# Kernel optimization log

Measured on AMD Instinct MI355X. Metric: run time of the kernel, lower is better.

## Reference

```python
import jax, jax.numpy as jnp
import numpy as np

N_NODES = 100000


def gcn_conv(x, W, b, src, dst, dinv):
    # PyG GCNConv with default add_self_loops=True, symmetric normalization.
    # x: [N, Fin], W: [Fin, Fout]. Self-loop contribution handled analytically
    # (norm for loop edge i->i is dinv[i]^2) instead of materializing loop edges.
    xw = x @ W                                   # [N, Fout]
    norm = dinv[src] * dinv[dst]                 # [E]
    msgs = xw[src] * norm[:, None]               # [E, Fout]
    agg = jax.ops.segment_sum(msgs, dst, num_segments=N_NODES)
    agg = agg + xw * (dinv * dinv)[:, None]      # self-loops
    return agg + b


def setup_inputs() -> dict:
    key = jax.random.key(0)
    ks = jax.random.split(key, 12)
    E = 3200000
    S = 1000000
    F_in = 512
    x = jax.random.normal(ks[0], (N_NODES, F_in), dtype=jnp.float32)
    edge_index = jax.random.randint(ks[1], (2, E), 0, N_NODES, dtype=jnp.int64)
    samples = jax.random.randint(ks[2], (S, 2), 0, N_NODES, dtype=jnp.int64)

    def glorot(k, fi, fo):
        lim = float(np.sqrt(6.0 / (fi + fo)))
        return jax.random.uniform(k, (fi, fo), jnp.float32, -lim, lim)

    W1 = glorot(ks[3], F_in, 8)
    b1 = jnp.zeros((8,), jnp.float32)
    W2 = glorot(ks[4], 8, 16)
    b2 = jnp.zeros((16,), jnp.float32)
    W3 = glorot(ks[5], 16, 32)
    b3 = jnp.zeros((32,), jnp.float32)
    Wfc = glorot(ks[6], 64, 1)
    bfc = jnp.zeros((1,), jnp.float32)
    return {"x": x, "edge_index": edge_index, "samples": samples,
            "W1": W1, "b1": b1, "W2": W2, "b2": b2, "W3": W3, "b3": b3,
            "Wfc": Wfc, "bfc": bfc}


def reference(x, edge_index, samples, W1, b1, W2, b2, W3, b3, Wfc, bfc):
    src, dst = edge_index[0], edge_index[1]
    # degree with self-loops (edge weight 1), deg >= 1 so rsqrt is safe
    deg = jax.ops.segment_sum(jnp.ones_like(src, dtype=x.dtype), dst,
                              num_segments=N_NODES) + 1.0
    dinv = jax.lax.rsqrt(deg)
    h = jax.nn.relu(gcn_conv(x, W1, b1, src, dst, dinv))
    h = jax.nn.relu(gcn_conv(h, W2, b2, src, dst, dinv))
    h = gcn_conv(h, W3, b3, src, dst, dinv)
    x_i = h[samples[:, 0]]                       # [S, 32]
    x_j = h[samples[:, 1]]                       # [S, 32]
    x_ij = jnp.concatenate([x_i, x_j], axis=1)   # [S, 64]
    return jax.nn.sigmoid(x_ij @ Wfc + bfc).squeeze(-1)
```

## Files before the change

kernel.cpp:

```cpp
#include <hip/hip_runtime.h>
#include <cstdint>

#define N_NODES 100000
#define NBKT 2048
#define KNODE 49
#define NBLK 256
#define TPB_P 512


__global__ void k_hist(const int* __restrict__ dst, int* __restrict__ hist, int E) {
    __shared__ int h[NBKT];
    for (int i = threadIdx.x; i < NBKT; i += blockDim.x) h[i] = 0;
    __syncthreads();
    int chunk = (E + NBLK - 1) / NBLK;
    int lo = blockIdx.x * chunk, hi = min(lo + chunk, E);
    for (int i = lo + threadIdx.x; i < hi; i += blockDim.x)
        atomicAdd(&h[dst[i] / KNODE], 1);
    __syncthreads();
    int* hr = hist + (size_t)blockIdx.x * NBKT;
    for (int i = threadIdx.x; i < NBKT; i += blockDim.x) hr[i] = h[i];
}


__global__ void k_offs(const int* __restrict__ hist, int* __restrict__ offs,
                       int* __restrict__ btot) {
    int bkt = blockIdx.x * blockDim.x + threadIdx.x;
    if (bkt >= NBKT) return;
    int run = 0;
    for (int rr = 0; rr < NBLK; ++rr) {
        int r = ((rr & 31) << 3) | (rr >> 5);
        int v = hist[(size_t)r * NBKT + bkt];
        offs[(size_t)r * NBKT + bkt] = run;
        run += v;
    }
    btot[bkt] = run;
}


__global__ void k_bktscan(const int* __restrict__ btot, int* __restrict__ bbase) {
    __shared__ int s[256];
    int t = threadIdx.x;
    int loc[8];
    int sum = 0;
#pragma unroll
    for (int j = 0; j < 8; ++j) { loc[j] = btot[t * 8 + j]; sum += loc[j]; }
    s[t] = sum;
    __syncthreads();
    for (int off = 1; off < 256; off <<= 1) {
        int v = (t >= off) ? s[t - off] : 0;
        __syncthreads();
        s[t] += v;
        __syncthreads();
    }
    int base = s[t] - sum;
#pragma unroll
    for (int j = 0; j < 8; ++j) { bbase[t * 8 + j] = base; base += loc[j]; }
    if (t == 255) bbase[NBKT] = base;
}


__global__ void k_place(const int* __restrict__ src, const int* __restrict__ dst,
                        const int* __restrict__ offs, const int* __restrict__ bbase,
                        int* __restrict__ tmp, int E) {
    __shared__ int cur[NBKT];
    const int* orow = offs + (size_t)blockIdx.x * NBKT;
    for (int i = threadIdx.x; i < NBKT; i += blockDim.x) cur[i] = bbase[i] + orow[i];
    __syncthreads();
    int chunk = (E + NBLK - 1) / NBLK;
    int lo = blockIdx.x * chunk, hi = min(lo + chunk, E);
    for (int i = lo + threadIdx.x; i < hi; i += blockDim.x) {
        int d = dst[i], s = src[i];
        int b = d / KNODE;
        int p = atomicAdd(&cur[b], 1);
        tmp[p] = (s << 6) | (d - b * KNODE);
    }
}


__global__ void k_countscan(const int* __restrict__ tmp, const int* __restrict__ bbase,
                            int* __restrict__ row_start, float* __restrict__ dinv, int n) {
    __shared__ int c[KNODE];
    __shared__ int p[KNODE];
    int b = blockIdx.x;
    int t = threadIdx.x;
    for (int i = t; i < KNODE; i += blockDim.x) c[i] = 0;
    __syncthreads();
    int n0 = bbase[b], n1 = bbase[b + 1];
    for (int i = n0 + t; i < n1; i += blockDim.x)
        atomicAdd(&c[tmp[i] & 63], 1);
    __syncthreads();
    if (t == 0) {
        int run = 0;
        for (int j = 0; j < KNODE; ++j) { p[j] = run; run += c[j]; }
    }
    __syncthreads();
    if (t < KNODE) {
        int node = b * KNODE + t;
        if (node < n) {
            row_start[node] = n0 + p[t];
            dinv[node] = rsqrtf((float)c[t] + 1.0f);
        }
    }
    if (b == 0 && t == 0) row_start[n] = bbase[NBKT];
}


__global__ void k_bin2(const int* __restrict__ tmp, const int* __restrict__ bbase,
                       const int* __restrict__ row_start, const float* __restrict__ dinv,
                       int2* __restrict__ csr, int n) {
    __shared__ int cur[KNODE];
    __shared__ float dd[KNODE];
    int b = blockIdx.x;
    int t = threadIdx.x;
    if (t < KNODE) {
        int node = b * KNODE + t;
        cur[t] = (node < n) ? row_start[node] : 0;
        dd[t] = (node < n) ? dinv[node] : 0.f;
    }
    __syncthreads();
    int n0 = bbase[b], n1 = bbase[b + 1];
    for (int i = n0 + t; i < n1; i += blockDim.x) {
        int e = tmp[i];
        int li = e & 63;
        int s = e >> 6;
        int pos = atomicAdd(&cur[li], 1);
        csr[pos] = make_int2(s, __float_as_int(dinv[s] * dd[li]));
    }
}


__global__ void k_gemm1(const float* __restrict__ x, const float* __restrict__ W,
                        float* __restrict__ xw, int n) {
    __shared__ float sWT[8 * 512];
    for (int i = threadIdx.x; i < 4096; i += blockDim.x) {
        int k = i >> 3, c = i & 7;
        sWT[c * 512 + k] = W[i];
    }
    __syncthreads();
    int wid = (blockIdx.x * blockDim.x + threadIdx.x) >> 6;
    int lane = threadIdx.x & 63;
    int r_sub = lane >> 3, j = lane & 7;
    int row = wid * 8 + r_sub;
    if (row >= n) return;
    const float* xr = x + (size_t)row * 512;
    float acc[8];
#pragma unroll
    for (int c = 0; c < 8; ++c) acc[c] = 0.f;
#pragma unroll 4
    for (int it = 0; it < 16; ++it) {
        int kb = it * 32 + j * 4;
        float4 v = *(const float4*)(xr + kb);
#pragma unroll
        for (int c = 0; c < 8; ++c) {
            const float* wt = &sWT[c * 512 + kb];
            acc[c] += v.x * wt[0] + v.y * wt[1] + v.z * wt[2] + v.w * wt[3];
        }
    }
#pragma unroll
    for (int off = 1; off < 8; off <<= 1)
#pragma unroll
        for (int c = 0; c < 8; ++c)
            acc[c] += __shfl_xor(acc[c], off);
    float outv = acc[0];
#pragma unroll
    for (int c = 1; c < 8; ++c) if (j == c) outv = acc[c];
    xw[(size_t)row * 8 + j] = outv;
}


__global__ void k_gather1(const float* __restrict__ xw, const int2* __restrict__ csr,
                          const int* __restrict__ row_start, const float* __restrict__ dinv,
                          const float* __restrict__ b, float* __restrict__ out, int n) {
    int wid = (blockIdx.x * blockDim.x + threadIdx.x) >> 6;
    int lane = threadIdx.x & 63;
    if (wid >= n) return;
    int e = lane >> 3, c = lane & 7;
    int k0 = row_start[wid], k1 = row_start[wid + 1];
    float acc = 0.f;
    for (int k = k0 + e; k < k1; k += 8) {
        int2 p = csr[k];
        acc += xw[(size_t)p.x * 8 + c] * __int_as_float(p.y);
    }
    if (e == 0) { float di = dinv[wid]; acc += xw[(size_t)wid * 8 + c] * di * di; }
#pragma unroll
    for (int off = 8; off < 64; off <<= 1) acc += __shfl_xor(acc, off);
    if (lane < 8) out[(size_t)wid * 8 + c] = fmaxf(acc + b[c], 0.f);
}


__global__ void k_gather2(const float* __restrict__ h1, const int2* __restrict__ csr,
                          const int* __restrict__ row_start, const float* __restrict__ dinv,
                          const float* __restrict__ W2, const float* __restrict__ b2,
                          float* __restrict__ h2, int n) {
    __shared__ float sW[8 * 16];
    __shared__ float sB[16];
    if (threadIdx.x < 128) sW[threadIdx.x] = W2[threadIdx.x];
    if (threadIdx.x < 16) sB[threadIdx.x] = b2[threadIdx.x];
    __syncthreads();
    int wid = (blockIdx.x * blockDim.x + threadIdx.x) >> 6;
    int lane = threadIdx.x & 63;
    if (wid >= n) return;
    int e = lane >> 3, c = lane & 7;
    int k0 = row_start[wid], k1 = row_start[wid + 1];
    float acc = 0.f;
    for (int k = k0 + e; k < k1; k += 8) {
        int2 p = csr[k];
        acc += h1[(size_t)p.x * 8 + c] * __int_as_float(p.y);
    }
    if (e == 0) { float di = dinv[wid]; acc += h1[(size_t)wid * 8 + c] * di * di; }
#pragma unroll
    for (int off = 8; off < 64; off <<= 1) acc += __shfl_xor(acc, off);
    float s2[8];
#pragma unroll
    for (int k = 0; k < 8; ++k) s2[k] = __shfl(acc, k);
    if (lane < 16) {
        float a = sB[lane];
#pragma unroll
        for (int k = 0; k < 8; ++k) a += s2[k] * sW[k * 16 + lane];
        h2[(size_t)wid * 16 + lane] = fmaxf(a, 0.f);
    }
}


__global__ void k_gather3(const float* __restrict__ h2, const int2* __restrict__ csr,
                          const int* __restrict__ row_start, const float* __restrict__ dinv,
                          const float* __restrict__ v, const float* __restrict__ ch,
                          float* __restrict__ pi, float* __restrict__ pj, int n) {
    int wid = (blockIdx.x * blockDim.x + threadIdx.x) >> 6;
    int lane = threadIdx.x & 63;
    if (wid >= n) return;
    int e = lane >> 4, c = lane & 15;
    int k0 = row_start[wid], k1 = row_start[wid + 1];
    float acc = 0.f;
    for (int k = k0 + e; k < k1; k += 4) {
        int2 p = csr[k];
        acc += h2[(size_t)p.x * 16 + c] * __int_as_float(p.y);
    }
    if (e == 0) { float di = dinv[wid]; acc += h2[(size_t)wid * 16 + c] * di * di; }
#pragma unroll
    for (int off = 16; off < 64; off <<= 1) acc += __shfl_xor(acc, off);
    float t = acc * v[c];
    float u = acc * v[16 + c];
#pragma unroll
    for (int off = 1; off < 16; off <<= 1) {
        t += __shfl_xor(t, off);
        u += __shfl_xor(u, off);
    }
    if (lane == 0) { pi[wid] = t + ch[0]; pj[wid] = u + ch[1]; }
}


__global__ void k_prep_head(const float* __restrict__ W3, const float* __restrict__ b3,
                            const float* __restrict__ Wfc, float* __restrict__ v,
                            float* __restrict__ c) {
    int t = threadIdx.x;
    if (t < 32) {
        int j = t & 15;
        const float* wf = Wfc + (t < 16 ? 0 : 32);
        float a = 0.f;
        for (int k = 0; k < 32; ++k) a += W3[j * 32 + k] * wf[k];
        v[t] = a;
    } else if (t < 34) {
        const float* wf = Wfc + (t == 32 ? 0 : 32);
        float a = 0.f;
        for (int k = 0; k < 32; ++k) a += b3[k] * wf[k];
        c[t - 32] = a;
    }
}


__global__ void k_samples_fast(const int2* __restrict__ samples, const float* __restrict__ pi,
                               const float* __restrict__ pj, const float* __restrict__ bfc,
                               float* __restrict__ out, int S) {
    int i = blockIdx.x * blockDim.x + threadIdx.x;
    if (i >= S) return;
    int2 s = samples[i];
    float z = pi[s.x] + pj[s.y] + bfc[0];
    out[i] = 1.0f / (1.0f + __expf(-z));
}


extern "C" void kernel_launch(void* const* d_in, const int* in_sizes, int n_in,
                              void* d_out, int out_size, void* d_ws, size_t ws_size,
                              hipStream_t stream) {
    const float* x   = (const float*)d_in[0];
    const int*   ei  = (const int*)d_in[1];
    const int*   smp = (const int*)d_in[2];
    const float* W1  = (const float*)d_in[3];
    const float* b1  = (const float*)d_in[4];
    const float* W2  = (const float*)d_in[5];
    const float* b2  = (const float*)d_in[6];
    const float* W3  = (const float*)d_in[7];
    const float* b3  = (const float*)d_in[8];
    const float* Wfc = (const float*)d_in[9];
    const float* bfc = (const float*)d_in[10];
    float* out = (float*)d_out;

    const int E = in_sizes[1] / 2;
    const int S = in_sizes[2] / 2;
    const int N = N_NODES;
    const int* src = ei;
    const int* dst = ei + E;

    char* w = (char*)d_ws;
    size_t off = 0;
    auto alloc = [&](size_t bytes) {
        char* p = w + off;
        off += (bytes + 255) & ~(size_t)255;
        return p;
    };
    int*   row_start = (int*)alloc((N + 1) * 4);
    float* dinv      = (float*)alloc(N * 4);
    int2*  csr       = (int2*)alloc((size_t)E * 8);
    int*   btot      = (int*)alloc(NBKT * 4);
    int*   bbase     = (int*)alloc((NBKT + 1) * 4);

    size_t off_layers = off;
    float* xw1       = (float*)alloc((size_t)N * 8 * 4);
    float* h1        = (float*)alloc((size_t)N * 8 * 4);
    float* h2        = (float*)alloc((size_t)N * 16 * 4);
    float* vhead     = (float*)alloc(32 * 4);
    float* chead     = (float*)alloc(2 * 4);
    float* pi        = (float*)alloc(N * 4);
    float* pj        = (float*)alloc(N * 4);

    size_t tmp_off  = off_layers;
    size_t hist_off = tmp_off + (((size_t)E * 4 + 255) & ~(size_t)255);
    size_t offs_off = hist_off + (((size_t)NBLK * NBKT * 4 + 255) & ~(size_t)255);
    int* tmp  = (int*)(w + tmp_off);
    int* hist = (int*)(w + hist_off);
    int* offs = (int*)(w + offs_off);
    size_t scratch_end = offs_off + (size_t)NBLK * NBKT * 4;
    if (scratch_end > off) off = (scratch_end + 255) & ~(size_t)255;

    dim3 B(256);
    const int GN = (N * 64 + 255) / 256;

    k_hist<<<dim3(NBLK), dim3(TPB_P), 0, stream>>>(dst, hist, E);
    k_offs<<<dim3((NBKT + 255) / 256), B, 0, stream>>>(hist, offs, btot);
    k_bktscan<<<dim3(1), B, 0, stream>>>(btot, bbase);
    k_place<<<dim3(NBLK), dim3(TPB_P), 0, stream>>>(src, dst, offs, bbase, tmp, E);
    k_countscan<<<dim3(NBKT), B, 0, stream>>>(tmp, bbase, row_start, dinv, N);
    k_bin2<<<dim3(NBKT), B, 0, stream>>>(tmp, bbase, row_start, dinv, csr, N);

    k_gemm1<<<dim3(((N + 7) / 8 * 64 + 255) / 256), B, 0, stream>>>(x, W1, xw1, N);
    k_gather1<<<dim3(GN), B, 0, stream>>>(xw1, csr, row_start, dinv, b1, h1, N);

    k_gather2<<<dim3(GN), B, 0, stream>>>(h1, csr, row_start, dinv, W2, b2, h2, N);

    k_prep_head<<<dim3(1), dim3(64), 0, stream>>>(W3, b3, Wfc, vhead, chead);
    k_gather3<<<dim3(GN), B, 0, stream>>>(h2, csr, row_start, dinv, vhead, chead, pi, pj, N);

    k_samples_fast<<<dim3((S + 255) / 256), B, 0, stream>>>((const int2*)smp, pi, pj, bfc, out, S);
}
```

Baseline: 638.4 us.

## Fold symmetric normalization into node features and drop per-edge weights from CSR

The per-edge norm dinv[s]*dinv[d] is factored: source features are pre-scaled by dinv when produced (in the GEMM and at each layer output), and the aggregate is scaled by dinv of the destination. This lets the CSR hold only 4-byte source indices instead of int2 (index, weight), halving edge-list traffic in all three gather passes and removing the dinv[s] random read at build time. The count and bin kernels are merged into one finalize kernel that caches bucket entries in shared memory, and the per-bucket offset scan is parallelised across a wavefront with shuffles. The cost is an extra multiply per node and reliance on the bucket size fitting the shared cache, with a fallback to global reads when it does not.

```diff
diff --git a/kernel.cpp b/kernel.cpp
--- a/kernel.cpp
+++ b/kernel.cpp
@@ -6,6 +6,7 @@
 #define KNODE 49
 #define NBLK 256
 #define TPB_P 512
+#define CAP  2048
 
 
 __global__ void k_hist(const int* __restrict__ dst, int* __restrict__ hist, int E) {
@@ -24,16 +25,33 @@
 
 __global__ void k_offs(const int* __restrict__ hist, int* __restrict__ offs,
                        int* __restrict__ btot) {
-    int bkt = blockIdx.x * blockDim.x + threadIdx.x;
+    int bkt = (blockIdx.x * blockDim.x + threadIdx.x) >> 6;
     if (bkt >= NBKT) return;
-    int run = 0;
-    for (int rr = 0; rr < NBLK; ++rr) {
+    int lane = threadIdx.x & 63;
+    int vals[4], loc[4];
+    int s = 0;
+#pragma unroll
+    for (int j = 0; j < 4; ++j) {
+        int rr = lane * 4 + j;
         int r = ((rr & 31) << 3) | (rr >> 5);
-        int v = hist[(size_t)r * NBKT + bkt];
-        offs[(size_t)r * NBKT + bkt] = run;
-        run += v;
-    }
-    btot[bkt] = run;
+        vals[j] = hist[(size_t)r * NBKT + bkt];
+        loc[j] = s;
+        s += vals[j];
+    }
+    int inc = s;
+#pragma unroll
+    for (int off = 1; off < 64; off <<= 1) {
+        int u = __shfl_up(inc, off);
+        if (lane >= off) inc += u;
+    }
+    int excl = inc - s;
+#pragma unroll
+    for (int j = 0; j < 4; ++j) {
+        int rr = lane * 4 + j;
+        int r = ((rr & 31) << 3) | (rr >> 5);
+        offs[(size_t)r * NBKT + bkt] = excl + loc[j];
+    }
+    if (lane == 63) btot[bkt] = excl + s;
 }
 
 
@@ -77,60 +95,50 @@
 }
 
 
-__global__ void k_countscan(const int* __restrict__ tmp, const int* __restrict__ bbase,
-                            int* __restrict__ row_start, float* __restrict__ dinv, int n) {
-    __shared__ int c[KNODE];
-    __shared__ int p[KNODE];
+__global__ void k_finalize(const int* __restrict__ tmp, const int* __restrict__ bbase,
+                           int* __restrict__ row_start, float* __restrict__ dinv,
+                           int* __restrict__ csr, int n) {
+    __shared__ int sE[CAP];
+    __shared__ int cnt[KNODE];
+    __shared__ int pfx[KNODE];
+    __shared__ int cur[KNODE];
     int b = blockIdx.x;
     int t = threadIdx.x;
-    for (int i = t; i < KNODE; i += blockDim.x) c[i] = 0;
+    for (int i = t; i < KNODE; i += blockDim.x) cnt[i] = 0;
     __syncthreads();
     int n0 = bbase[b], n1 = bbase[b + 1];
-    for (int i = n0 + t; i < n1; i += blockDim.x)
-        atomicAdd(&c[tmp[i] & 63], 1);
+    int m = n1 - n0;
+    for (int i = t; i < m; i += blockDim.x) {
+        int e = tmp[n0 + i];
+        if (i < CAP) sE[i] = e;
+        atomicAdd(&cnt[e & 63], 1);
+    }
     __syncthreads();
     if (t == 0) {
-        int run = 0;
-        for (int j = 0; j < KNODE; ++j) { p[j] = run; run += c[j]; }
+        int run = n0;
+        for (int j = 0; j < KNODE; ++j) { pfx[j] = run; run += cnt[j]; }
     }
     __syncthreads();
     if (t < KNODE) {
         int node = b * KNODE + t;
         if (node < n) {
-            row_start[node] = n0 + p[t];
-            dinv[node] = rsqrtf((float)c[t] + 1.0f);
+            row_start[node] = pfx[t];
+            dinv[node] = rsqrtf((float)cnt[t] + 1.0f);
         }
+        cur[t] = pfx[t];
     }
     if (b == 0 && t == 0) row_start[n] = bbase[NBKT];
-}
-
-
-__global__ void k_bin2(const int* __restrict__ tmp, const int* __restrict__ bbase,
-                       const int* __restrict__ row_start, const float* __restrict__ dinv,
-                       int2* __restrict__ csr, int n) {
-    __shared__ int cur[KNODE];
-    __shared__ float dd[KNODE];
-    int b = blockIdx.x;
-    int t = threadIdx.x;
-    if (t < KNODE) {
-        int node = b * KNODE + t;
-        cur[t] = (node < n) ? row_start[node] : 0;
-        dd[t] = (node < n) ? dinv[node] : 0.f;
-    }
-    __syncthreads();
-    int n0 = bbase[b], n1 = bbase[b + 1];
-    for (int i = n0 + t; i < n1; i += blockDim.x) {
-        int e = tmp[i];
-        int li = e & 63;
-        int s = e >> 6;
-        int pos = atomicAdd(&cur[li], 1);
-        csr[pos] = make_int2(s, __float_as_int(dinv[s] * dd[li]));
+    __syncthreads();
+    for (int i = t; i < m; i += blockDim.x) {
+        int e = (i < CAP) ? sE[i] : tmp[n0 + i];
+        int pos = atomicAdd(&cur[e & 63], 1);
+        csr[pos] = e >> 6;
     }
 }
 
 
 __global__ void k_gemm1(const float* __restrict__ x, const float* __restrict__ W,
-                        float* __restrict__ xw, int n) {
+                        const float* __restrict__ dinv, float* __restrict__ xw, int n) {
     __shared__ float sWT[8 * 512];
     for (int i = threadIdx.x; i < 4096; i += blockDim.x) {
         int k = i >> 3, c = i & 7;
@@ -164,11 +172,11 @@
     float outv = acc[0];
 #pragma unroll
     for (int c = 1; c < 8; ++c) if (j == c) outv = acc[c];
-    xw[(size_t)row * 8 + j] = outv;
-}
-
-
-__global__ void k_gather1(const float* __restrict__ xw, const int2* __restrict__ csr,
+    xw[(size_t)row * 8 + j] = outv * dinv[row];
+}
+
+
+__global__ void k_gather1(const float* __restrict__ xw, const int* __restrict__ csr,
                           const int* __restrict__ row_start, const float* __restrict__ dinv,
                           const float* __restrict__ b, float* __restrict__ out, int n) {
     int wid = (blockIdx.x * blockDim.x + threadIdx.x) >> 6;
@@ -177,18 +185,19 @@
     int e = lane >> 3, c = lane & 7;
     int k0 = row_start[wid], k1 = row_start[wid + 1];
     float acc = 0.f;
-    for (int k = k0 + e; k < k1; k += 8) {
-        int2 p = csr[k];
-        acc += xw[(size_t)p.x * 8 + c] * __int_as_float(p.y);
-    }
-    if (e == 0) { float di = dinv[wid]; acc += xw[(size_t)wid * 8 + c] * di * di; }
+    for (int k = k0 + e; k < k1; k += 8)
+        acc += xw[(size_t)csr[k] * 8 + c];
+    if (e == 0) acc += xw[(size_t)wid * 8 + c];
 #pragma unroll
     for (int off = 8; off < 64; off <<= 1) acc += __shfl_xor(acc, off);
-    if (lane < 8) out[(size_t)wid * 8 + c] = fmaxf(acc + b[c], 0.f);
-}
-
-
-__global__ void k_gather2(const float* __restrict__ h1, const int2* __restrict__ csr,
+    if (lane < 8) {
+        float di = dinv[wid];
+        out[(size_t)wid * 8 + c] = fmaxf(acc * di + b[c], 0.f) * di;
+    }
+}
+
+
+__global__ void k_gather2(const float* __restrict__ h1, const int* __restrict__ csr,
                           const int* __restrict__ row_start, const float* __restrict__ dinv,
                           const float* __restrict__ W2, const float* __restrict__ b2,
                           float* __restrict__ h2, int n) {
@@ -203,13 +212,13 @@
     int e = lane >> 3, c = lane & 7;
     int k0 = row_start[wid], k1 = row_start[wid + 1];
     float acc = 0.f;
-    for (int k = k0 + e; k < k1; k += 8) {
-        int2 p = csr[k];
-        acc += h1[(size_t)p.x * 8 + c] * __int_as_float(p.y);
-    }
-    if (e == 0) { float di = dinv[wid]; acc += h1[(size_t)wid * 8 + c] * di * di; }
+    for (int k = k0 + e; k < k1; k += 8)
+        acc += h1[(size_t)csr[k] * 8 + c];
+    if (e == 0) acc += h1[(size_t)wid * 8 + c];
 #pragma unroll
     for (int off = 8; off < 64; off <<= 1) acc += __shfl_xor(acc, off);
+    float di = dinv[wid];
+    acc *= di;
     float s2[8];
 #pragma unroll
     for (int k = 0; k < 8; ++k) s2[k] = __shfl(acc, k);
@@ -217,12 +226,12 @@
         float a = sB[lane];
 #pragma unroll
         for (int k = 0; k < 8; ++k) a += s2[k] * sW[k * 16 + lane];
-        h2[(size_t)wid * 16 + lane] = fmaxf(a, 0.f);
-    }
-}
-
-
-__global__ void k_gather3(const float* __restrict__ h2, const int2* __restrict__ csr,
+        h2[(size_t)wid * 16 + lane] = fmaxf(a, 0.f) * di;
+    }
+}
+
+
+__global__ void k_gather3(const float* __restrict__ h2, const int* __restrict__ csr,
                           const int* __restrict__ row_start, const float* __restrict__ dinv,
                           const float* __restrict__ v, const float* __restrict__ ch,
                           float* __restrict__ pi, float* __restrict__ pj, int n) {
@@ -232,11 +241,9 @@
     int e = lane >> 4, c = lane & 15;
     int k0 = row_start[wid], k1 = row_start[wid + 1];
     float acc = 0.f;
-    for (int k = k0 + e; k < k1; k += 4) {
-        int2 p = csr[k];
-        acc += h2[(size_t)p.x * 16 + c] * __int_as_float(p.y);
-    }
-    if (e == 0) { float di = dinv[wid]; acc += h2[(size_t)wid * 16 + c] * di * di; }
+    for (int k = k0 + e; k < k1; k += 4)
+        acc += h2[(size_t)csr[k] * 16 + c];
+    if (e == 0) acc += h2[(size_t)wid * 16 + c];
 #pragma unroll
     for (int off = 16; off < 64; off <<= 1) acc += __shfl_xor(acc, off);
     float t = acc * v[c];
@@ -246,7 +253,11 @@
         t += __shfl_xor(t, off);
         u += __shfl_xor(u, off);
     }
-    if (lane == 0) { pi[wid] = t + ch[0]; pj[wid] = u + ch[1]; }
+    if (lane == 0) {
+        float di = dinv[wid];
+        pi[wid] = t * di + ch[0];
+        pj[wid] = u * di + ch[1];
+    }
 }
 
 
@@ -311,7 +322,7 @@
     };
     int*   row_start = (int*)alloc((N + 1) * 4);
     float* dinv      = (float*)alloc(N * 4);
-    int2*  csr       = (int2*)alloc((size_t)E * 8);
+    int*   csr       = (int*)alloc((size_t)E * 4);
     int*   btot      = (int*)alloc(NBKT * 4);
     int*   bbase     = (int*)alloc((NBKT + 1) * 4);
 
@@ -337,13 +348,12 @@
     const int GN = (N * 64 + 255) / 256;
 
     k_hist<<<dim3(NBLK), dim3(TPB_P), 0, stream>>>(dst, hist, E);
-    k_offs<<<dim3((NBKT + 255) / 256), B, 0, stream>>>(hist, offs, btot);
+    k_offs<<<dim3(NBKT * 64 / 256), B, 0, stream>>>(hist, offs, btot);
     k_bktscan<<<dim3(1), B, 0, stream>>>(btot, bbase);
     k_place<<<dim3(NBLK), dim3(TPB_P), 0, stream>>>(src, dst, offs, bbase, tmp, E);
-    k_countscan<<<dim3(NBKT), B, 0, stream>>>(tmp, bbase, row_start, dinv, N);
-    k_bin2<<<dim3(NBKT), B, 0, stream>>>(tmp, bbase, row_start, dinv, csr, N);
-
-    k_gemm1<<<dim3(((N + 7) / 8 * 64 + 255) / 256), B, 0, stream>>>(x, W1, xw1, N);
+    k_finalize<<<dim3(NBKT), B, 0, stream>>>(tmp, bbase, row_start, dinv, csr, N);
+
+    k_gemm1<<<dim3(((N + 7) / 8 * 64 + 255) / 256), B, 0, stream>>>(x, W1, dinv, xw1, N);
     k_gather1<<<dim3(GN), B, 0, stream>>>(xw1, csr, row_start, dinv, b1, h1, N);
 
     k_gather2<<<dim3(GN), B, 0, stream>>>(h1, csr, row_start, dinv, W2, b2, h2, N);
```

Result: faster. 611.9 us (-4.1%).
